# Kernel optimization log

Measured on AMD Instinct MI355X. Metric: run time of the kernel, lower is better.

The kernel has to match this reference:

```python
import jax, jax.numpy as jnp
import numpy as np

D = 128   # latent_dim
H = 128   # mlp_hidden_dim
S = 2     # message_passing_steps
NM = 30000   # mesh nodes
NO = 2000    # obj nodes
EMM = 240000 # mesh->mesh edges
EMO = 60000  # mesh->obj edges


def _ln(h, g, b):
    m = jnp.mean(h, axis=-1, keepdims=True)
    v = jnp.mean((h - m) ** 2, axis=-1, keepdims=True)
    return (h - m) * jax.lax.rsqrt(v + 1e-5) * g + b


def _mlp_ln(h, W0, b0, W1, b1, W2, b2, g, bt):
    # build_mlp(in, [H]*2, out) + LayerNorm(out)
    h = jax.nn.relu(h @ W0 + b0)
    h = jax.nn.relu(h @ W1 + b1)
    h = h @ W2 + b2
    return _ln(h, g, bt)


def _edge_conv(x_src, x_dst, ei, ea, W0, b0, W1, b1, W2, b2, g, bt):
    # PyG source_to_target: x_j = src gather (ei[0]), x_i = dst gather (ei[1])
    xi = x_dst[ei[1]]
    xj = x_src[ei[0]]
    msg = _mlp_ln(jnp.concatenate([xi, xj, ea], axis=-1), W0, b0, W1, b1, W2, b2, g, bt)
    aggr = jax.ops.segment_sum(msg, ei[1], num_segments=x_dst.shape[0])
    return ea + msg, aggr  # residual on edge attr; aggr is sum of raw messages


def _node_conv(x, aggr, W0, b0, W1, b1, W2, b2, g, bt):
    return x + _mlp_ln(jnp.concatenate([x, aggr], axis=-1), W0, b0, W1, b1, W2, b2, g, bt)


def setup_inputs() -> dict:
    key = jax.random.key(0)
    ks = jax.random.split(key, 16)
    f = jnp.float32
    x_mesh = jax.random.normal(ks[0], (NM, D), f)
    x_obj = jax.random.normal(ks[1], (NO, D), f)
    ea_mm = jax.random.normal(ks[2], (EMM, D), f)
    ea_mo = jax.random.normal(ks[3], (EMO, D), f)
    ei_mm = jnp.stack([jax.random.randint(ks[4], (EMM,), 0, NM),
                       jax.random.randint(ks[5], (EMM,), 0, NM)]).astype(jnp.int32)
    ei_mo = jnp.stack([jax.random.randint(ks[6], (EMO,), 0, NM),
                       jax.random.randint(ks[7], (EMO,), 0, NO)]).astype(jnp.int32)

    def w(k, shape, fan):
        return jax.random.normal(k, shape, f) * (1.0 / np.sqrt(fan))

    # params stacked as [edge_or_node_type(2), step(S), ...]
    eW0 = w(ks[8], (2, S, 3 * D, H), 3 * D); eb0 = jnp.zeros((2, S, H), f)
    eW1 = w(ks[9], (2, S, H, H), H);         eb1 = jnp.zeros((2, S, H), f)
    eW2 = w(ks[10], (2, S, H, D), H);        eb2 = jnp.zeros((2, S, D), f)
    eg = jnp.ones((2, S, D), f);             ebt = jnp.zeros((2, S, D), f)
    nW0 = w(ks[11], (2, S, 2 * D, H), 2 * D); nb0 = jnp.zeros((2, S, H), f)
    nW1 = w(ks[12], (2, S, H, H), H);         nb1 = jnp.zeros((2, S, H), f)
    nW2 = w(ks[13], (2, S, H, D), H);         nb2 = jnp.zeros((2, S, D), f)
    ng = jnp.ones((2, S, D), f);              nbt = jnp.zeros((2, S, D), f)
    return dict(x_mesh=x_mesh, x_obj=x_obj, ei_mm=ei_mm, ei_mo=ei_mo,
                ea_mm=ea_mm, ea_mo=ea_mo,
                eW0=eW0, eb0=eb0, eW1=eW1, eb1=eb1, eW2=eW2, eb2=eb2, eg=eg, ebt=ebt,
                nW0=nW0, nb0=nb0, nW1=nW1, nb1=nb1, nW2=nW2, nb2=nb2, ng=ng, nbt=nbt)


def reference(x_mesh, x_obj, ei_mm, ei_mo, ea_mm, ea_mo,
              eW0, eb0, eW1, eb1, eW2, eb2, eg, ebt,
              nW0, nb0, nW1, nb1, nW2, nb2, ng, nbt):
    for s in range(S):
        ep = lambda t: (eW0[t, s], eb0[t, s], eW1[t, s], eb1[t, s], eW2[t, s], eb2[t, s], eg[t, s], ebt[t, s])
        npar = lambda t: (nW0[t, s], nb0[t, s], nW1[t, s], nb1[t, s], nW2[t, s], nb2[t, s], ng[t, s], nbt[t, s])
        # edge convs use node features at layer input
        ea_mm, agg_mesh = _edge_conv(x_mesh, x_mesh, ei_mm, ea_mm, *ep(0))
        ea_mo, agg_obj = _edge_conv(x_mesh, x_obj, ei_mo, ea_mo, *ep(1))
        x_mesh = _node_conv(x_mesh, agg_mesh, *npar(0))
        x_obj = _node_conv(x_obj, agg_obj, *npar(1))
    return (x_mesh, x_obj)
```

## Files before the change

kernel.cpp:

```cpp
#include <hip/hip_runtime.h>

#define DD 128
#define NMESH 30000
#define NOBJ 2000
#define EMMN 240000
#define EMON 60000
#define NB_MM (EMMN / 64)
#define NB_MO ((EMON + 63) / 64)
#define NB_NM ((NMESH + 63) / 64)
#define NB_NO ((NOBJ + 63) / 64)

typedef unsigned short u16;
typedef short short8 __attribute__((ext_vector_type(8)));
typedef float f32x4 __attribute__((ext_vector_type(4)));
typedef __bf16 bf16x8 __attribute__((ext_vector_type(8)));

union FragCvt { short8 s; bf16x8 b; };

static __device__ __forceinline__ u16 f2bf(float f) {
  union { float f; unsigned u; } v; v.f = f;
  unsigned r = v.u + 0x7FFFu + ((v.u >> 16) & 1u);
  return (u16)(r >> 16);
}
static __device__ __forceinline__ float bf2f(u16 u) {
  union { unsigned u; float f; } v; v.u = ((unsigned)u) << 16; return v.f;
}
static __device__ __forceinline__ int swz256(int row, int b) {
  return row * 256 + (b ^ ((row & 7) << 4));
}
static __device__ __forceinline__ bf16x8 ldsFrag(const u16* s, int row, int kByte) {
  FragCvt u; u.s = *(const short8*)((const char*)s + swz256(row, kByte));
  return u.b;
}

static __device__ __forceinline__ void ld_w(short8 w[8], const u16* W, int rowLen,
                                            int colOff, int wrow, int wh) {
  const u16* g = W + (size_t)wrow * rowLen + colOff + wh * 64;
  #pragma unroll
  for (int j = 0; j < 8; ++j) w[j] = *(const short8*)(g + j * 8);
}
static __device__ __forceinline__ void wr_w(u16* sW, const short8 w[8], int wrow, int wh) {
  #pragma unroll
  for (int j = 0; j < 8; ++j)
    *(short8*)((char*)sW + swz256(wrow, wh * 128 + j * 16)) = w[j];
}
static __device__ __forceinline__ void ld_rows_bf(short8 a[4], const u16* src, int seg) {
  #pragma unroll
  for (int j = 0; j < 4; ++j) a[j] = *(const short8*)(src + seg * 32 + j * 8);
}
static __device__ __forceinline__ void wr_rows(u16* sIn, const short8 a[4], int row, int seg) {
  #pragma unroll
  for (int j = 0; j < 4; ++j)
    *(short8*)((char*)sIn + swz256(row, seg * 64 + j * 16)) = a[j];
}
static __device__ __forceinline__ void ld_rows_f32cvt(short8 a[4], const float* src, int seg) {
  #pragma unroll
  for (int j = 0; j < 4; ++j) {
    f32x4 f0 = *(const f32x4*)(src + seg * 32 + j * 8);
    f32x4 f1 = *(const f32x4*)(src + seg * 32 + j * 8 + 4);
    #pragma unroll
    for (int q = 0; q < 4; ++q) { a[j][q] = (short)f2bf(f0[q]); a[j][4 + q] = (short)f2bf(f1[q]); }
  }
}

static __device__ __forceinline__ void mfma_128k(const u16* sIn, const u16* sW,
                                                 int wr, int wc, int lrow, int lk,
                                                 f32x4 acc[2][4]) {
  #pragma unroll
  for (int kc = 0; kc < 4; ++kc) {
    bf16x8 a0 = ldsFrag(sIn, wr * 32 + lrow, kc * 64 + lk * 16);
    bf16x8 a1 = ldsFrag(sIn, wr * 32 + 16 + lrow, kc * 64 + lk * 16);
    #pragma unroll
    for (int ct = 0; ct < 4; ++ct) {
      bf16x8 b = ldsFrag(sW, wc * 64 + ct * 16 + lrow, kc * 64 + lk * 16);
      acc[0][ct] = __builtin_amdgcn_mfma_f32_16x16x32_bf16(a0, b, acc[0][ct], 0, 0, 0);
      acc[1][ct] = __builtin_amdgcn_mfma_f32_16x16x32_bf16(a1, b, acc[1][ct], 0, 0, 0);
    }
  }
}

static __device__ __forceinline__ void transition_relu(u16* sIn, const float* sBias, int biasOff,
                                                       int wr, int wc, int lrow, int lk,
                                                       f32x4 acc[2][4]) {
  #pragma unroll
  for (int rt = 0; rt < 2; ++rt) {
    #pragma unroll
    for (int ct = 0; ct < 4; ++ct) {
      const int col = wc * 64 + ct * 16 + lrow;
      const float bias = sBias[biasOff + col];
      #pragma unroll
      for (int r = 0; r < 4; ++r) {
        const int orow = wr * 32 + rt * 16 + lk * 4 + r;
        float v = acc[rt][ct][r] + bias;
        v = fmaxf(v, 0.f);
        *(u16*)((char*)sIn + swz256(orow, col * 2)) = f2bf(v);
        acc[rt][ct][r] = 0.f;
      }
    }
  }
}

static __device__ __forceinline__ void ln_to_sIn(u16* sIn, float* sPart, const float* sBias,
                                                 int wr, int wc, int lrow, int lk,
                                                 f32x4 acc[2][4]) {
  float gv[4], bv[4];
  #pragma unroll
  for (int ct = 0; ct < 4; ++ct) {
    const int col = wc * 64 + ct * 16 + lrow;
    gv[ct] = sBias[384 + col];
    bv[ct] = sBias[512 + col];
  }
  float s1[2][4], s2[2][4];
  #pragma unroll
  for (int rt = 0; rt < 2; ++rt) {
    #pragma unroll
    for (int r = 0; r < 4; ++r) {
      float a = 0.f, b = 0.f;
      #pragma unroll
      for (int ct = 0; ct < 4; ++ct) {
        const int col = wc * 64 + ct * 16 + lrow;
        const float v = acc[rt][ct][r] + sBias[256 + col];
        acc[rt][ct][r] = v;
        a += v; b += v * v;
      }
      #pragma unroll
      for (int m = 1; m < 16; m <<= 1) { a += __shfl_xor(a, m); b += __shfl_xor(b, m); }
      s1[rt][r] = a; s2[rt][r] = b;
    }
  }
  if (lrow == 0) {
    #pragma unroll
    for (int rt = 0; rt < 2; ++rt)
      #pragma unroll
      for (int r = 0; r < 4; ++r) {
        const int e = wr * 32 + rt * 16 + lk * 4 + r;
        sPart[(wc * 64 + e) * 2] = s1[rt][r];
        sPart[(wc * 64 + e) * 2 + 1] = s2[rt][r];
      }
  }
  __syncthreads();
  #pragma unroll
  for (int rt = 0; rt < 2; ++rt)
    #pragma unroll
    for (int r = 0; r < 4; ++r) {
      const int e = wr * 32 + rt * 16 + lk * 4 + r;
      const float t1 = s1[rt][r] + sPart[((1 - wc) * 64 + e) * 2];
      const float t2 = s2[rt][r] + sPart[((1 - wc) * 64 + e) * 2 + 1];
      const float m = t1 * (1.f / 128.f);
      const float var = t2 * (1.f / 128.f) - m * m;
      const float rstd = rsqrtf(var + 1e-5f);
      #pragma unroll
      for (int ct = 0; ct < 4; ++ct) {
        const int col = wc * 64 + ct * 16 + lrow;
        const float ln = (acc[rt][ct][r] - m) * rstd * gv[ct] + bv[ct];
        *(u16*)((char*)sIn + swz256(e, col * 2)) = f2bf(ln);
      }
    }
}

static __device__ void edge_body(int bid,
    const u16* xsrc, const u16* xdst, const int* ei, int E,
    const float* ea_f32, u16* ea_bf,
    const u16* W0T, const u16* W1T, const u16* W2T,
    const float* b0, const float* b1, const float* b2,
    const float* gq, const float* btq, u16* msg_out,
    u16* sIn, u16* sW, float* sBias, float* sPart)
{
  const int tid = threadIdx.x;
  const int wave = tid >> 6, lane = tid & 63;
  const int lrow = lane & 15, lk = lane >> 4;
  const int wr = wave >> 1, wc = wave & 1;
  const int e0 = bid * 64;
  const int row = tid >> 2, seg = tid & 3;
  const int eRow = (e0 + row < E) ? (e0 + row) : (E - 1);
  const int wrow = tid >> 1, wh = tid & 1;
  const bool eaf = (ea_f32 != nullptr);

  if (tid < 128) {
    sBias[tid] = b0[tid];
    sBias[128 + tid] = b1[tid];
    sBias[256 + tid] = b2[tid];
    sBias[384 + tid] = gq[tid];
    sBias[512 + tid] = btq[tid];
  }

  const f32x4 zero = {0.f, 0.f, 0.f, 0.f};
  f32x4 acc[2][4];
  #pragma unroll
  for (int i = 0; i < 2; ++i)
    #pragma unroll
    for (int j = 0; j < 4; ++j) acc[i][j] = zero;

  short8 w[8], a[4];
  short8 eaReg[4];

  ld_w(w, W0T, 384, 0, wrow, wh);
  { const int idx = ei[E + eRow]; ld_rows_bf(a, xdst + (size_t)idx * DD, seg); }
  wr_w(sW, w, wrow, wh);
  wr_rows(sIn, a, row, seg);
  ld_w(w, W0T, 384, 128, wrow, wh);
  { const int idx = ei[eRow]; ld_rows_bf(a, xsrc + (size_t)idx * DD, seg); }
  __syncthreads();
  mfma_128k(sIn, sW, wr, wc, lrow, lk, acc);
  __syncthreads();

  wr_w(sW, w, wrow, wh);
  wr_rows(sIn, a, row, seg);
  ld_w(w, W0T, 384, 256, wrow, wh);
  if (eaf) ld_rows_f32cvt(eaReg, ea_f32 + (size_t)eRow * DD, seg);
  else     ld_rows_bf(eaReg, ea_bf + (size_t)eRow * DD, seg);
  __syncthreads();
  mfma_128k(sIn, sW, wr, wc, lrow, lk, acc);
  __syncthreads();

  wr_w(sW, w, wrow, wh);
  wr_rows(sIn, eaReg, row, seg);
  ld_w(w, W1T, 128, 0, wrow, wh);
  __syncthreads();
  mfma_128k(sIn, sW, wr, wc, lrow, lk, acc);
  __syncthreads();

  transition_relu(sIn, sBias, 0, wr, wc, lrow, lk, acc);
  wr_w(sW, w, wrow, wh);
  ld_w(w, W2T, 128, 0, wrow, wh);
  __syncthreads();
  mfma_128k(sIn, sW, wr, wc, lrow, lk, acc);
  __syncthreads();

  transition_relu(sIn, sBias, 128, wr, wc, lrow, lk, acc);
  wr_w(sW, w, wrow, wh);
  __syncthreads();
  mfma_128k(sIn, sW, wr, wc, lrow, lk, acc);
  __syncthreads();

  ln_to_sIn(sIn, sPart, sBias, wr, wc, lrow, lk, acc);
  __syncthreads();

  const int e = e0 + row;
  if (e < E) {
    short8 msgv[4];
    #pragma unroll
    for (int j = 0; j < 4; ++j)
      msgv[j] = *(const short8*)((const char*)sIn + swz256(row, seg * 64 + j * 16));
    u16* msgRow = msg_out + (size_t)e * DD + seg * 32;
    u16* eaRow  = ea_bf + (size_t)e * DD + seg * 32;
    #pragma unroll
    for (int j = 0; j < 4; ++j) {
      short8 en;
      #pragma unroll
      for (int q = 0; q < 8; ++q)
        en[q] = (short)f2bf(bf2f((u16)eaReg[j][q]) + bf2f((u16)msgv[j][q]));
      *(short8*)(eaRow + j * 8) = en;
      *(short8*)(msgRow + j * 8) = msgv[j];
    }
  }
}

__global__ __launch_bounds__(256, 2) void edge_conv_kernel(
    const u16* __restrict__ xm_bf, const u16* __restrict__ xo_bf,
    const int* __restrict__ ei_mm, const int* __restrict__ ei_mo,
    const float* __restrict__ eaf_mm, const float* __restrict__ eaf_mo,
    u16* __restrict__ eab_mm, u16* __restrict__ eab_mo,
    const u16* __restrict__ W0a, const u16* __restrict__ W1a, const u16* __restrict__ W2a,
    const u16* __restrict__ W0b, const u16* __restrict__ W1b, const u16* __restrict__ W2b,
    const float* __restrict__ b0a, const float* __restrict__ b1a, const float* __restrict__ b2a,
    const float* __restrict__ ga, const float* __restrict__ bta,
    const float* __restrict__ b0b, const float* __restrict__ b1b, const float* __restrict__ b2b,
    const float* __restrict__ gb, const float* __restrict__ btb,
    u16* __restrict__ msg_mm, u16* __restrict__ msg_mo)
{
  __shared__ u16 sIn[64 * 128];
  __shared__ u16 sW[128 * 128];
  __shared__ float sBias[5 * 128];
  __shared__ float sPart[2 * 64 * 2];
  if ((int)blockIdx.x < NB_MM)
    edge_body(blockIdx.x, xm_bf, xm_bf, ei_mm, EMMN, eaf_mm, eab_mm,
              W0a, W1a, W2a, b0a, b1a, b2a, ga, bta, msg_mm, sIn, sW, sBias, sPart);
  else
    edge_body(blockIdx.x - NB_MM, xm_bf, xo_bf, ei_mo, EMON, eaf_mo, eab_mo,
              W0b, W1b, W2b, b0b, b1b, b2b, gb, btb, msg_mo, sIn, sW, sBias, sPart);
}

static __device__ void node_body(int bid, u16* x_bf, const float* aggin, float* x_f32, int N,
    const u16* W0T, const u16* W1T, const u16* W2T,
    const float* b0, const float* b1, const float* b2,
    const float* gq, const float* btq,
    u16* sIn, u16* sW, float* sBias, float* sPart)
{
  const int tid = threadIdx.x;
  const int wave = tid >> 6, lane = tid & 63;
  const int lrow = lane & 15, lk = lane >> 4;
  const int wr = wave >> 1, wc = wave & 1;
  const int n0 = bid * 64;
  const int row = tid >> 2, seg = tid & 3;
  const int nRow = (n0 + row < N) ? (n0 + row) : (N - 1);
  const int wrow = tid >> 1, wh = tid & 1;

  if (tid < 128) {
    sBias[tid] = b0[tid];
    sBias[128 + tid] = b1[tid];
    sBias[256 + tid] = b2[tid];
    sBias[384 + tid] = gq[tid];
    sBias[512 + tid] = btq[tid];
  }

  const f32x4 zero = {0.f, 0.f, 0.f, 0.f};
  f32x4 acc[2][4];
  #pragma unroll
  for (int i = 0; i < 2; ++i)
    #pragma unroll
    for (int j = 0; j < 4; ++j) acc[i][j] = zero;

  short8 w[8], a[4];

  ld_w(w, W0T, 256, 0, wrow, wh);
  ld_rows_bf(a, x_bf + (size_t)nRow * DD, seg);
  wr_w(sW, w, wrow, wh);
  wr_rows(sIn, a, row, seg);
  ld_w(w, W0T, 256, 128, wrow, wh);
  ld_rows_f32cvt(a, aggin + (size_t)nRow * DD, seg);
  __syncthreads();
  mfma_128k(sIn, sW, wr, wc, lrow, lk, acc);
  __syncthreads();

  wr_w(sW, w, wrow, wh);
  wr_rows(sIn, a, row, seg);
  ld_w(w, W1T, 128, 0, wrow, wh);
  __syncthreads();
  mfma_128k(sIn, sW, wr, wc, lrow, lk, acc);
  __syncthreads();

  transition_relu(sIn, sBias, 0, wr, wc, lrow, lk, acc);
  wr_w(sW, w, wrow, wh);
  ld_w(w, W2T, 128, 0, wrow, wh);
  __syncthreads();
  mfma_128k(sIn, sW, wr, wc, lrow, lk, acc);
  __syncthreads();

  transition_relu(sIn, sBias, 128, wr, wc, lrow, lk, acc);
  wr_w(sW, w, wrow, wh);
  __syncthreads();
  mfma_128k(sIn, sW, wr, wc, lrow, lk, acc);
  __syncthreads();

  ln_to_sIn(sIn, sPart, sBias, wr, wc, lrow, lk, acc);
  __syncthreads();

  const int n = n0 + row;
  if (n < N) {
    short8 lnv[4];
    #pragma unroll
    for (int j = 0; j < 4; ++j)
      lnv[j] = *(const short8*)((const char*)sIn + swz256(row, seg * 64 + j * 16));
    float* xr = x_f32 + (size_t)n * DD + seg * 32;
    u16* xb = x_bf + (size_t)n * DD + seg * 32;
    #pragma unroll
    for (int j = 0; j < 4; ++j) {
      f32x4 o0 = *(const f32x4*)(xr + j * 8);
      f32x4 o1 = *(const f32x4*)(xr + j * 8 + 4);
      f32x4 n0v, n1v;
      short8 pb;
      #pragma unroll
      for (int q = 0; q < 4; ++q) {
        n0v[q] = o0[q] + bf2f((u16)lnv[j][q]);
        n1v[q] = o1[q] + bf2f((u16)lnv[j][4 + q]);
        pb[q]     = (short)f2bf(n0v[q]);
        pb[4 + q] = (short)f2bf(n1v[q]);
      }
      *(f32x4*)(xr + j * 8) = n0v;
      *(f32x4*)(xr + j * 8 + 4) = n1v;
      *(short8*)(xb + j * 8) = pb;
    }
  }
}

__global__ __launch_bounds__(256, 2) void node_conv_kernel(
    u16* __restrict__ xm_bf, u16* __restrict__ xo_bf,
    const float* __restrict__ agg_m, const float* __restrict__ agg_o,
    float* __restrict__ xf_m, float* __restrict__ xf_o,
    const u16* __restrict__ W0a, const u16* __restrict__ W1a, const u16* __restrict__ W2a,
    const u16* __restrict__ W0b, const u16* __restrict__ W1b, const u16* __restrict__ W2b,
    const float* __restrict__ b0a, const float* __restrict__ b1a, const float* __restrict__ b2a,
    const float* __restrict__ ga, const float* __restrict__ bta,
    const float* __restrict__ b0b, const float* __restrict__ b1b, const float* __restrict__ b2b,
    const float* __restrict__ gb, const float* __restrict__ btb)
{
  __shared__ u16 sIn[64 * 128];
  __shared__ u16 sW[128 * 128];
  __shared__ float sBias[5 * 128];
  __shared__ float sPart[2 * 64 * 2];
  if ((int)blockIdx.x < NB_NM)
    node_body(blockIdx.x, xm_bf, agg_m, xf_m, NMESH,
              W0a, W1a, W2a, b0a, b1a, b2a, ga, bta, sIn, sW, sBias, sPart);
  else
    node_body(blockIdx.x - NB_NM, xo_bf, agg_o, xf_o, NOBJ,
              W0b, W1b, W2b, b0b, b1b, b2b, gb, btb, sIn, sW, sBias, sPart);
}

__global__ void hist_kernel(const int* __restrict__ ei_mm, const int* __restrict__ ei_mo,
                            int* __restrict__ deg_m, int* __restrict__ deg_o) {
  int i = blockIdx.x * blockDim.x + threadIdx.x;
  if (i < EMMN) atomicAdd(&deg_m[ei_mm[EMMN + i]], 1);
  else { int j = i - EMMN; if (j < EMON) atomicAdd(&deg_o[ei_mo[EMON + j]], 1); }
}

__global__ __launch_bounds__(1024) void scan_kernel(
    const int* __restrict__ deg_m, int* __restrict__ start_m, int* __restrict__ cur_m,
    const int* __restrict__ deg_o, int* __restrict__ start_o, int* __restrict__ cur_o) {
  const int* deg; int* start; int* cursor; int N;
  if (blockIdx.x == 0) { deg = deg_m; start = start_m; cursor = cur_m; N = NMESH; }
  else                 { deg = deg_o; start = start_o; cursor = cur_o; N = NOBJ; }
  __shared__ int lds[1024];
  const int t = threadIdx.x;
  const int chunk = (N + 1023) >> 10;
  const int base = t * chunk;
  const int end = min(base + chunk, N);
  int s = 0;
  for (int i = base; i < end; ++i) s += deg[i];
  lds[t] = s;
  __syncthreads();
  for (int d = 1; d < 1024; d <<= 1) {
    int v = (t >= d) ? lds[t - d] : 0;
    __syncthreads();
    lds[t] += v;
    __syncthreads();
  }
  int off = lds[t] - s;
  for (int i = base; i < end; ++i) { start[i] = off; cursor[i] = off; off += deg[i]; }
  if (t == 1023) start[N] = lds[1023];
}

__global__ void scatter_kernel(const int* __restrict__ ei_mm, const int* __restrict__ ei_mo,
                               int* __restrict__ cur_m, int* __restrict__ cur_o,
                               int* __restrict__ perm_m, int* __restrict__ perm_o) {
  int i = blockIdx.x * blockDim.x + threadIdx.x;
  if (i < EMMN) { int p = atomicAdd(&cur_m[ei_mm[EMMN + i]], 1); perm_m[p] = i; }
  else { int j = i - EMMN; if (j < EMON) { int p = atomicAdd(&cur_o[ei_mo[EMON + j]], 1); perm_o[p] = j; } }
}

__global__ __launch_bounds__(256) void agg_gather_kernel(
    const u16* __restrict__ msg_m, const int* __restrict__ start_m, const int* __restrict__ perm_m,
    float* __restrict__ agg_m,
    const u16* __restrict__ msg_o, const int* __restrict__ start_o, const int* __restrict__ perm_o,
    float* __restrict__ agg_o)
{
  const int wave = threadIdx.x >> 6, lane = threadIdx.x & 63;
  int idx = blockIdx.x * 4 + wave;
  const u16* msg; const int* start; const int* perm; float* agg; int n;
  if (idx < NMESH) { msg = msg_m; start = start_m; perm = perm_m; agg = agg_m; n = idx; }
  else {
    n = idx - NMESH;
    if (n >= NOBJ) return;
    msg = msg_o; start = start_o; perm = perm_o; agg = agg_o;
  }
  const int i0 = start[n], i1 = start[n + 1];
  float a0 = 0.f, a1 = 0.f;
  int i = i0;
  for (; i + 1 < i1; i += 2) {
    const int e1 = perm[i], e2 = perm[i + 1];
    unsigned v1 = *(const unsigned*)(msg + (size_t)e1 * DD + lane * 2);
    unsigned v2 = *(const unsigned*)(msg + (size_t)e2 * DD + lane * 2);
    a0 += bf2f((u16)(v1 & 0xFFFFu)) + bf2f((u16)(v2 & 0xFFFFu));
    a1 += bf2f((u16)(v1 >> 16)) + bf2f((u16)(v2 >> 16));
  }
  if (i < i1) {
    const int e1 = perm[i];
    unsigned v1 = *(const unsigned*)(msg + (size_t)e1 * DD + lane * 2);
    a0 += bf2f((u16)(v1 & 0xFFFFu));
    a1 += bf2f((u16)(v1 >> 16));
  }
  float* ar = agg + (size_t)n * DD + lane * 2;
  ar[0] = a0;
  ar[1] = a1;
}

static __device__ __forceinline__ void wcvt(const float* src, u16* dst, int K, int b, int t) {
  int i = b * 256 + t;
  int n = i & 127;
  int k = (i >> 7) % K;
  int sl = i / (K * 128);
  dst[((size_t)sl * 128 + n) * K + k] = f2bf(src[i]);
}

__global__ void prep_kernel(
    const float* __restrict__ eW0, const float* __restrict__ eW1, const float* __restrict__ eW2,
    const float* __restrict__ nW0, const float* __restrict__ nW1, const float* __restrict__ nW2,
    u16* __restrict__ eW0T, u16* __restrict__ eW1T, u16* __restrict__ eW2T,
    u16* __restrict__ nW0T, u16* __restrict__ nW1T, u16* __restrict__ nW2T,
    int* __restrict__ deg_m, int* __restrict__ deg_o,
    const float* __restrict__ xm, const float* __restrict__ xo,
    float* __restrict__ xf, u16* __restrict__ xmb, u16* __restrict__ xob)
{
  const int b = blockIdx.x, t = threadIdx.x;
  if (b < 768)        wcvt(eW0, eW0T, 384, b, t);
  else if (b < 1024)  wcvt(eW1, eW1T, 128, b - 768, t);
  else if (b < 1280)  wcvt(eW2, eW2T, 128, b - 1024, t);
  else if (b < 1792)  wcvt(nW0, nW0T, 256, b - 1280, t);
  else if (b < 2048)  wcvt(nW1, nW1T, 128, b - 1792, t);
  else if (b < 2304)  wcvt(nW2, nW2T, 128, b - 2048, t);
  else if (b < 2429) {
    int i = (b - 2304) * 256 + t;
    if (i < NMESH) deg_m[i] = 0;
    else if (i < NMESH + NOBJ) deg_o[i - NMESH] = 0;
  } else {
    int i = (b - 2429) * 256 + t;
    const int tm = NMESH * DD;
    if (i < tm) { float v = xm[i]; xf[i] = v; xmb[i] = f2bf(v); }
    else { int j = i - tm; float v = xo[j]; xf[tm + j] = v; xob[j] = f2bf(v); }
  }
}

extern "C" void kernel_launch(void* const* d_in, const int* in_sizes, int n_in,
                              void* d_out, int out_size, void* d_ws, size_t ws_size,
                              hipStream_t stream)
{
  const float* x_mesh = (const float*)d_in[0];
  const float* x_obj  = (const float*)d_in[1];
  const int*   ei_mm  = (const int*)d_in[2];
  const int*   ei_mo  = (const int*)d_in[3];
  const float* ea_mm  = (const float*)d_in[4];
  const float* ea_mo  = (const float*)d_in[5];
  const float* eW0 = (const float*)d_in[6];
  const float* eb0 = (const float*)d_in[7];
  const float* eW1 = (const float*)d_in[8];
  const float* eb1 = (const float*)d_in[9];
  const float* eW2 = (const float*)d_in[10];
  const float* eb2 = (const float*)d_in[11];
  const float* eg  = (const float*)d_in[12];
  const float* ebt = (const float*)d_in[13];
  const float* nW0 = (const float*)d_in[14];
  const float* nb0 = (const float*)d_in[15];
  const float* nW1 = (const float*)d_in[16];
  const float* nb1 = (const float*)d_in[17];
  const float* nW2 = (const float*)d_in[18];
  const float* nb2 = (const float*)d_in[19];
  const float* ng  = (const float*)d_in[20];
  const float* nbt = (const float*)d_in[21];

  u16* eamm_bf = (u16*)d_ws;
  u16* eamo_bf = eamm_bf + (size_t)EMMN * DD;
  u16* xm_bf   = eamo_bf + (size_t)EMON * DD;
  u16* xo_bf   = xm_bf + (size_t)NMESH * DD;
  float* agg_m = (float*)(xo_bf + (size_t)NOBJ * DD);
  float* agg_o = agg_m + (size_t)NMESH * DD;
  u16* eW0T = (u16*)(agg_o + (size_t)NOBJ * DD);
  u16* eW1T = eW0T + (size_t)4 * 128 * 384;
  u16* eW2T = eW1T + (size_t)4 * 128 * 128;
  u16* nW0T = eW2T + (size_t)4 * 128 * 128;
  u16* nW1T = nW0T + (size_t)4 * 128 * 256;
  u16* nW2T = nW1T + (size_t)4 * 128 * 128;
  u16* msg_mm = nW2T + (size_t)4 * 128 * 128;
  u16* msg_mo = msg_mm + (size_t)EMMN * DD;
  int* deg_m   = (int*)(msg_mo + (size_t)EMON * DD);
  int* start_m = deg_m + NMESH;
  int* cur_m   = start_m + NMESH + 1;
  int* perm_mm = cur_m + NMESH;
  int* deg_o   = perm_mm + EMMN;
  int* start_o = deg_o + NOBJ;
  int* cur_o   = start_o + NOBJ + 1;
  int* perm_mo = cur_o + NOBJ;

  float* xf_m = (float*)d_out;
  float* xf_o = xf_m + (size_t)NMESH * DD;

  prep_kernel<<<18429, 256, 0, stream>>>(eW0, eW1, eW2, nW0, nW1, nW2,
                                         eW0T, eW1T, eW2T, nW0T, nW1T, nW2T,
                                         deg_m, deg_o, x_mesh, x_obj, xf_m, xm_bf, xo_bf);
  hist_kernel<<<(EMMN + EMON + 255) / 256, 256, 0, stream>>>(ei_mm, ei_mo, deg_m, deg_o);
  scan_kernel<<<2, 1024, 0, stream>>>(deg_m, start_m, cur_m, deg_o, start_o, cur_o);
  scatter_kernel<<<(EMMN + EMON + 255) / 256, 256, 0, stream>>>(ei_mm, ei_mo, cur_m, cur_o,
                                                                perm_mm, perm_mo);

  for (int s = 0; s < 2; ++s) {
    const int sa = 0 * 2 + s, sb = 1 * 2 + s;
    edge_conv_kernel<<<NB_MM + NB_MO, 256, 0, stream>>>(
        xm_bf, xo_bf, ei_mm, ei_mo,
        (s == 0) ? ea_mm : (const float*)nullptr,
        (s == 0) ? ea_mo : (const float*)nullptr,
        eamm_bf, eamo_bf,
        eW0T + (size_t)sa * 128 * 384, eW1T + (size_t)sa * 128 * 128, eW2T + (size_t)sa * 128 * 128,
        eW0T + (size_t)sb * 128 * 384, eW1T + (size_t)sb * 128 * 128, eW2T + (size_t)sb * 128 * 128,
        eb0 + sa * 128, eb1 + sa * 128, eb2 + sa * 128, eg + sa * 128, ebt + sa * 128,
        eb0 + sb * 128, eb1 + sb * 128, eb2 + sb * 128, eg + sb * 128, ebt + sb * 128,
        msg_mm, msg_mo);
    agg_gather_kernel<<<(NMESH + NOBJ + 3) / 4, 256, 0, stream>>>(
        msg_mm, start_m, perm_mm, agg_m, msg_mo, start_o, perm_mo, agg_o);
    node_conv_kernel<<<NB_NM + NB_NO, 256, 0, stream>>>(
        xm_bf, xo_bf, agg_m, agg_o, xf_m, xf_o,
        nW0T + (size_t)sa * 128 * 256, nW1T + (size_t)sa * 128 * 128, nW2T + (size_t)sa * 128 * 128,
        nW0T + (size_t)sb * 128 * 256, nW1T + (size_t)sb * 128 * 128, nW2T + (size_t)sb * 128 * 128,
        nb0 + sa * 128, nb1 + sa * 128, nb2 + sa * 128, ng + sa * 128, nbt + sa * 128,
        nb0 + sb * 128, nb1 + sb * 128, nb2 + sb * 128, ng + sb * 128, nbt + sb * 128);
  }
}
```

Measured before the change: 771.5 us.

## Load MFMA operands directly from global memory, dropping LDS weight staging

```diff
diff --git a/kernel.cpp b/kernel.cpp
--- a/kernel.cpp
+++ b/kernel.cpp
@@ -32,47 +32,70 @@
   FragCvt u; u.s = *(const short8*)((const char*)s + swz256(row, kByte));
   return u.b;
 }
-
-static __device__ __forceinline__ void ld_w(short8 w[8], const u16* W, int rowLen,
-                                            int colOff, int wrow, int wh) {
-  const u16* g = W + (size_t)wrow * rowLen + colOff + wh * 64;
-  #pragma unroll
-  for (int j = 0; j < 8; ++j) w[j] = *(const short8*)(g + j * 8);
-}
-static __device__ __forceinline__ void wr_w(u16* sW, const short8 w[8], int wrow, int wh) {
-  #pragma unroll
-  for (int j = 0; j < 8; ++j)
-    *(short8*)((char*)sW + swz256(wrow, wh * 128 + j * 16)) = w[j];
-}
-static __device__ __forceinline__ void ld_rows_bf(short8 a[4], const u16* src, int seg) {
-  #pragma unroll
-  for (int j = 0; j < 4; ++j) a[j] = *(const short8*)(src + seg * 32 + j * 8);
-}
-static __device__ __forceinline__ void wr_rows(u16* sIn, const short8 a[4], int row, int seg) {
-  #pragma unroll
-  for (int j = 0; j < 4; ++j)
-    *(short8*)((char*)sIn + swz256(row, seg * 64 + j * 16)) = a[j];
-}
-static __device__ __forceinline__ void ld_rows_f32cvt(short8 a[4], const float* src, int seg) {
-  #pragma unroll
-  for (int j = 0; j < 4; ++j) {
-    f32x4 f0 = *(const f32x4*)(src + seg * 32 + j * 8);
-    f32x4 f1 = *(const f32x4*)(src + seg * 32 + j * 8 + 4);
-    #pragma unroll
-    for (int q = 0; q < 4; ++q) { a[j][q] = (short)f2bf(f0[q]); a[j][4 + q] = (short)f2bf(f1[q]); }
-  }
-}
-
-static __device__ __forceinline__ void mfma_128k(const u16* sIn, const u16* sW,
-                                                 int wr, int wc, int lrow, int lk,
-                                                 f32x4 acc[2][4]) {
+static __device__ __forceinline__ bf16x8 gFrag(const u16* p) {
+  FragCvt u; u.s = *(const short8*)(p);
+  return u.b;
+}
+
+static __device__ __forceinline__ void mfma_gg(const u16* a0p, const u16* a1p,
+    const u16* W, int rowLen, int colOff, int wcolBase, int lk,
+    f32x4 acc[2][4]) {
+  const u16* bp  = W + (size_t)wcolBase * rowLen + colOff + lk * 8;
+  const u16* ap0 = a0p + lk * 8;
+  const u16* ap1 = a1p + lk * 8;
+  #pragma unroll
+  for (int kc = 0; kc < 4; ++kc) {
+    bf16x8 a0 = gFrag(ap0 + kc * 32);
+    bf16x8 a1 = gFrag(ap1 + kc * 32);
+    #pragma unroll
+    for (int ct = 0; ct < 4; ++ct) {
+      bf16x8 b = gFrag(bp + (size_t)ct * 16 * rowLen + kc * 32);
+      acc[0][ct] = __builtin_amdgcn_mfma_f32_16x16x32_bf16(a0, b, acc[0][ct], 0, 0, 0);
+      acc[1][ct] = __builtin_amdgcn_mfma_f32_16x16x32_bf16(a1, b, acc[1][ct], 0, 0, 0);
+    }
+  }
+}
+
+static __device__ __forceinline__ void mfma_gg_f32A(const float* a0p, const float* a1p,
+    const u16* W, int rowLen, int colOff, int wcolBase, int lk,
+    f32x4 acc[2][4]) {
+  const u16* bp = W + (size_t)wcolBase * rowLen + colOff + lk * 8;
+  #pragma unroll
+  for (int kc = 0; kc < 4; ++kc) {
+    bf16x8 a0, a1;
+    {
+      f32x4 f0 = *(const f32x4*)(a0p + kc * 32 + lk * 8);
+      f32x4 f1 = *(const f32x4*)(a0p + kc * 32 + lk * 8 + 4);
+      f32x4 g0 = *(const f32x4*)(a1p + kc * 32 + lk * 8);
+      f32x4 g1 = *(const f32x4*)(a1p + kc * 32 + lk * 8 + 4);
+      FragCvt c0, c1;
+      #pragma unroll
+      for (int q = 0; q < 4; ++q) {
+        c0.s[q] = (short)f2bf(f0[q]); c0.s[4 + q] = (short)f2bf(f1[q]);
+        c1.s[q] = (short)f2bf(g0[q]); c1.s[4 + q] = (short)f2bf(g1[q]);
+      }
+      a0 = c0.b; a1 = c1.b;
+    }
+    #pragma unroll
+    for (int ct = 0; ct < 4; ++ct) {
+      bf16x8 b = gFrag(bp + (size_t)ct * 16 * rowLen + kc * 32);
+      acc[0][ct] = __builtin_amdgcn_mfma_f32_16x16x32_bf16(a0, b, acc[0][ct], 0, 0, 0);
+      acc[1][ct] = __builtin_amdgcn_mfma_f32_16x16x32_bf16(a1, b, acc[1][ct], 0, 0, 0);
+    }
+  }
+}
+
+static __device__ __forceinline__ void mfma_lg(const u16* sIn,
+    const u16* W, int rowLen, int wr, int wcolBase, int lrow, int lk,
+    f32x4 acc[2][4]) {
+  const u16* bp = W + (size_t)wcolBase * rowLen + lk * 8;
   #pragma unroll
   for (int kc = 0; kc < 4; ++kc) {
     bf16x8 a0 = ldsFrag(sIn, wr * 32 + lrow, kc * 64 + lk * 16);
     bf16x8 a1 = ldsFrag(sIn, wr * 32 + 16 + lrow, kc * 64 + lk * 16);
     #pragma unroll
     for (int ct = 0; ct < 4; ++ct) {
-      bf16x8 b = ldsFrag(sW, wc * 64 + ct * 16 + lrow, kc * 64 + lk * 16);
+      bf16x8 b = gFrag(bp + (size_t)ct * 16 * rowLen + kc * 32);
       acc[0][ct] = __builtin_amdgcn_mfma_f32_16x16x32_bf16(a0, b, acc[0][ct], 0, 0, 0);
       acc[1][ct] = __builtin_amdgcn_mfma_f32_16x16x32_bf16(a1, b, acc[1][ct], 0, 0, 0);
     }
@@ -164,16 +187,15 @@
     const u16* W0T, const u16* W1T, const u16* W2T,
     const float* b0, const float* b1, const float* b2,
     const float* gq, const float* btq, u16* msg_out,
-    u16* sIn, u16* sW, float* sBias, float* sPart)
+    u16* sIn, float* sBias, float* sPart, int* sIdx)
 {
   const int tid = threadIdx.x;
   const int wave = tid >> 6, lane = tid & 63;
   const int lrow = lane & 15, lk = lane >> 4;
   const int wr = wave >> 1, wc = wave & 1;
+  const int wcol = wc * 64 + lrow;
   const int e0 = bid * 64;
   const int row = tid >> 2, seg = tid & 3;
-  const int eRow = (e0 + row < E) ? (e0 + row) : (E - 1);
-  const int wrow = tid >> 1, wh = tid & 1;
   const bool eaf = (ea_f32 != nullptr);
 
   if (tid < 128) {
@@ -183,6 +205,12 @@
     sBias[384 + tid] = gq[tid];
     sBias[512 + tid] = btq[tid];
   }
+  if (tid < 64) {
+    int e = e0 + tid; if (e >= E) e = E - 1;
+    sIdx[tid] = ei[e];
+    sIdx[64 + tid] = ei[E + e];
+  }
+  __syncthreads();
 
   const f32x4 zero = {0.f, 0.f, 0.f, 0.f};
   f32x4 acc[2][4];
@@ -191,47 +219,28 @@
     #pragma unroll
     for (int j = 0; j < 4; ++j) acc[i][j] = zero;
 
-  short8 w[8], a[4];
-  short8 eaReg[4];
-
-  ld_w(w, W0T, 384, 0, wrow, wh);
-  { const int idx = ei[E + eRow]; ld_rows_bf(a, xdst + (size_t)idx * DD, seg); }
-  wr_w(sW, w, wrow, wh);
-  wr_rows(sIn, a, row, seg);
-  ld_w(w, W0T, 384, 128, wrow, wh);
-  { const int idx = ei[eRow]; ld_rows_bf(a, xsrc + (size_t)idx * DD, seg); }
-  __syncthreads();
-  mfma_128k(sIn, sW, wr, wc, lrow, lk, acc);
-  __syncthreads();
-
-  wr_w(sW, w, wrow, wh);
-  wr_rows(sIn, a, row, seg);
-  ld_w(w, W0T, 384, 256, wrow, wh);
-  if (eaf) ld_rows_f32cvt(eaReg, ea_f32 + (size_t)eRow * DD, seg);
-  else     ld_rows_bf(eaReg, ea_bf + (size_t)eRow * DD, seg);
-  __syncthreads();
-  mfma_128k(sIn, sW, wr, wc, lrow, lk, acc);
-  __syncthreads();
-
-  wr_w(sW, w, wrow, wh);
-  wr_rows(sIn, eaReg, row, seg);
-  ld_w(w, W1T, 128, 0, wrow, wh);
-  __syncthreads();
-  mfma_128k(sIn, sW, wr, wc, lrow, lk, acc);
-  __syncthreads();
+  const int r0 = wr * 32 + lrow, r1 = r0 + 16;
+  const int er0 = (e0 + r0 < E) ? (e0 + r0) : (E - 1);
+  const int er1 = (e0 + r1 < E) ? (e0 + r1) : (E - 1);
+
+  mfma_gg(xdst + (size_t)sIdx[64 + r0] * DD, xdst + (size_t)sIdx[64 + r1] * DD,
+          W0T, 384, 0, wcol, lk, acc);
+  mfma_gg(xsrc + (size_t)sIdx[r0] * DD, xsrc + (size_t)sIdx[r1] * DD,
+          W0T, 384, 128, wcol, lk, acc);
+  if (eaf)
+    mfma_gg_f32A(ea_f32 + (size_t)er0 * DD, ea_f32 + (size_t)er1 * DD,
+                 W0T, 384, 256, wcol, lk, acc);
+  else
+    mfma_gg(ea_bf + (size_t)er0 * DD, ea_bf + (size_t)er1 * DD,
+            W0T, 384, 256, wcol, lk, acc);
 
   transition_relu(sIn, sBias, 0, wr, wc, lrow, lk, acc);
-  wr_w(sW, w, wrow, wh);
-  ld_w(w, W2T, 128, 0, wrow, wh);
-  __syncthreads();
-  mfma_128k(sIn, sW, wr, wc, lrow, lk, acc);
-  __syncthreads();
-
+  __syncthreads();
+  mfma_lg(sIn, W1T, 128, wr, wcol, lrow, lk, acc);
+  __syncthreads();
   transition_relu(sIn, sBias, 128, wr, wc, lrow, lk, acc);
-  wr_w(sW, w, wrow, wh);
-  __syncthreads();
-  mfma_128k(sIn, sW, wr, wc, lrow, lk, acc);
-  __syncthreads();
+  __syncthreads();
+  mfma_lg(sIn, W2T, 128, wr, wcol, lrow, lk, acc);
 
   ln_to_sIn(sIn, sPart, sBias, wr, wc, lrow, lk, acc);
   __syncthreads();
@@ -244,14 +253,32 @@
       msgv[j] = *(const short8*)((const char*)sIn + swz256(row, seg * 64 + j * 16));
     u16* msgRow = msg_out + (size_t)e * DD + seg * 32;
     u16* eaRow  = ea_bf + (size_t)e * DD + seg * 32;
-    #pragma unroll
-    for (int j = 0; j < 4; ++j) {
-      short8 en;
-      #pragma unroll
-      for (int q = 0; q < 8; ++q)
-        en[q] = (short)f2bf(bf2f((u16)eaReg[j][q]) + bf2f((u16)msgv[j][q]));
-      *(short8*)(eaRow + j * 8) = en;
-      *(short8*)(msgRow + j * 8) = msgv[j];
+    if (eaf) {
+      const float* er = ea_f32 + (size_t)e * DD + seg * 32;
+      #pragma unroll
+      for (int j = 0; j < 4; ++j) {
+        f32x4 o0 = *(const f32x4*)(er + j * 8);
+        f32x4 o1 = *(const f32x4*)(er + j * 8 + 4);
+        short8 en;
+        #pragma unroll
+        for (int q = 0; q < 4; ++q) {
+          en[q]     = (short)f2bf(o0[q] + bf2f((u16)msgv[j][q]));
+          en[4 + q] = (short)f2bf(o1[q] + bf2f((u16)msgv[j][4 + q]));
+        }
+        *(short8*)(eaRow + j * 8) = en;
+        *(short8*)(msgRow + j * 8) = msgv[j];
+      }
+    } else {
+      #pragma unroll
+      for (int j = 0; j < 4; ++j) {
+        short8 old = *(const short8*)(eaRow + j * 8);
+        short8 en;
+        #pragma unroll
+        for (int q = 0; q < 8; ++q)
+          en[q] = (short)f2bf(bf2f((u16)old[q]) + bf2f((u16)msgv[j][q]));
+        *(short8*)(eaRow + j * 8) = en;
+        *(short8*)(msgRow + j * 8) = msgv[j];
+      }
     }
   }
 }
@@ -270,31 +297,30 @@
     u16* __restrict__ msg_mm, u16* __restrict__ msg_mo)
 {
   __shared__ u16 sIn[64 * 128];
-  __shared__ u16 sW[128 * 128];
   __shared__ float sBias[5 * 128];
   __shared__ float sPart[2 * 64 * 2];
+  __shared__ int sIdx[128];
   if ((int)blockIdx.x < NB_MM)
     edge_body(blockIdx.x, xm_bf, xm_bf, ei_mm, EMMN, eaf_mm, eab_mm,
-              W0a, W1a, W2a, b0a, b1a, b2a, ga, bta, msg_mm, sIn, sW, sBias, sPart);
+              W0a, W1a, W2a, b0a, b1a, b2a, ga, bta, msg_mm, sIn, sBias, sPart, sIdx);
   else
     edge_body(blockIdx.x - NB_MM, xm_bf, xo_bf, ei_mo, EMON, eaf_mo, eab_mo,
-              W0b, W1b, W2b, b0b, b1b, b2b, gb, btb, msg_mo, sIn, sW, sBias, sPart);
+              W0b, W1b, W2b, b0b, b1b, b2b, gb, btb, msg_mo, sIn, sBias, sPart, sIdx);
 }
 
 static __device__ void node_body(int bid, u16* x_bf, const float* aggin, float* x_f32, int N,
     const u16* W0T, const u16* W1T, const u16* W2T,
     const float* b0, const float* b1, const float* b2,
     const float* gq, const float* btq,
-    u16* sIn, u16* sW, float* sBias, float* sPart)
+    u16* sIn, float* sBias, float* sPart)
 {
   const int tid = threadIdx.x;
   const int wave = tid >> 6, lane = tid & 63;
   const int lrow = lane & 15, lk = lane >> 4;
   const int wr = wave >> 1, wc = wave & 1;
+  const int wcol = wc * 64 + lrow;
   const int n0 = bid * 64;
   const int row = tid >> 2, seg = tid & 3;
-  const int nRow = (n0 + row < N) ? (n0 + row) : (N - 1);
-  const int wrow = tid >> 1, wh = tid & 1;
 
   if (tid < 128) {
     sBias[tid] = b0[tid];
@@ -303,6 +329,7 @@
     sBias[384 + tid] = gq[tid];
     sBias[512 + tid] = btq[tid];
   }
+  __syncthreads();
 
   const f32x4 zero = {0.f, 0.f, 0.f, 0.f};
   f32x4 acc[2][4];
@@ -311,37 +338,22 @@
     #pragma unroll
     for (int j = 0; j < 4; ++j) acc[i][j] = zero;
 
-  short8 w[8], a[4];
-
-  ld_w(w, W0T, 256, 0, wrow, wh);
-  ld_rows_bf(a, x_bf + (size_t)nRow * DD, seg);
-  wr_w(sW, w, wrow, wh);
-  wr_rows(sIn, a, row, seg);
-  ld_w(w, W0T, 256, 128, wrow, wh);
-  ld_rows_f32cvt(a, aggin + (size_t)nRow * DD, seg);
-  __syncthreads();
-  mfma_128k(sIn, sW, wr, wc, lrow, lk, acc);
-  __syncthreads();
-
-  wr_w(sW, w, wrow, wh);
-  wr_rows(sIn, a, row, seg);
-  ld_w(w, W1T, 128, 0, wrow, wh);
-  __syncthreads();
-  mfma_128k(sIn, sW, wr, wc, lrow, lk, acc);
-  __syncthreads();
+  const int r0 = wr * 32 + lrow, r1 = r0 + 16;
+  const int nr0 = (n0 + r0 < N) ? (n0 + r0) : (N - 1);
+  const int nr1 = (n0 + r1 < N) ? (n0 + r1) : (N - 1);
+
+  mfma_gg(x_bf + (size_t)nr0 * DD, x_bf + (size_t)nr1 * DD,
+          W0T, 256, 0, wcol, lk, acc);
+  mfma_gg_f32A(aggin + (size_t)nr0 * DD, aggin + (size_t)nr1 * DD,
+               W0T, 256, 128, wcol, lk, acc);
 
   transition_relu(sIn, sBias, 0, wr, wc, lrow, lk, acc);
-  wr_w(sW, w, wrow, wh);
-  ld_w(w, W2T, 128, 0, wrow, wh);
-  __syncthreads();
-  mfma_128k(sIn, sW, wr, wc, lrow, lk, acc);
-  __syncthreads();
-
+  __syncthreads();
+  mfma_lg(sIn, W1T, 128, wr, wcol, lrow, lk, acc);
+  __syncthreads();
   transition_relu(sIn, sBias, 128, wr, wc, lrow, lk, acc);
-  wr_w(sW, w, wrow, wh);
-  __syncthreads();
-  mfma_128k(sIn, sW, wr, wc, lrow, lk, acc);
-  __syncthreads();
+  __syncthreads();
+  mfma_lg(sIn, W2T, 128, wr, wcol, lrow, lk, acc);
 
   ln_to_sIn(sIn, sPart, sBias, wr, wc, lrow, lk, acc);
   __syncthreads();
@@ -386,15 +398,14 @@
     const float* __restrict__ gb, const float* __restrict__ btb)
 {
   __shared__ u16 sIn[64 * 128];
-  __shared__ u16 sW[128 * 128];
   __shared__ float sBias[5 * 128];
   __shared__ float sPart[2 * 64 * 2];
   if ((int)blockIdx.x < NB_NM)
     node_body(blockIdx.x, xm_bf, agg_m, xf_m, NMESH,
-              W0a, W1a, W2a, b0a, b1a, b2a, ga, bta, sIn, sW, sBias, sPart);
+              W0a, W1a, W2a, b0a, b1a, b2a, ga, bta, sIn, sBias, sPart);
   else
     node_body(blockIdx.x - NB_NM, xo_bf, agg_o, xf_o, NOBJ,
-              W0b, W1b, W2b, b0b, b1b, b2b, gb, btb, sIn, sW, sBias, sPart);
+              W0b, W1b, W2b, b0b, b1b, b2b, gb, btb, sIn, sBias, sPart);
 }
 
 __global__ void hist_kernel(const int* __restrict__ ei_mm, const int* __restrict__ ei_mo,
```

Result: slower. 857.1 us (median of 2 runs) (+11.1%).
